# Performance work log

Measured on AMD Instinct MI355X. Metric: run time of the kernel, lower is better.

The kernel has to match this reference:

```python
import jax, jax.numpy as jnp
import numpy as np

KH = KW = 3
SH = SW = 1
PH = PW = 1
DH = DW = 1


def _median_pool2d(x):
    # x: (B, C, H, W); zero padding like F.unfold
    B, C, H, W = x.shape
    Ho = (H + 2 * PH - DH * (KH - 1) - 1) // SH + 1
    Wo = (W + 2 * PW - DW * (KW - 1) - 1) // SW + 1
    xp = jnp.pad(x, ((0, 0), (0, 0), (PH, PH), (PW, PW)))
    # gather kH*kW shifted strided views instead of materializing unfold copies per column
    wins = jnp.stack(
        [
            xp[:, :,
               i * DH: i * DH + (Ho - 1) * SH + 1: SH,
               j * DW: j * DW + (Wo - 1) * SW + 1: SW]
            for i in range(KH) for j in range(KW)
        ],
        axis=2,
    )  # (B, C, KH*KW, Ho, Wo)
    # torch.median returns the LOWER median: sorted element at index (n-1)//2
    s = jnp.sort(wins, axis=2)
    return s[:, :, (KH * KW - 1) // 2]


def setup_inputs() -> dict:
    key = jax.random.key(0)
    x = jax.random.normal(key, (8, 64, 256, 256), dtype=jnp.float32)
    return {"x": x}


def reference(x):
    return _median_pool2d(x)
```

## Files before the change

### kernel.cpp

```cpp
#include <hip/hip_runtime.h>
#include <hip/hip_bf16.h>


typedef float vf4 __attribute__((ext_vector_type(4)));

__device__ __forceinline__ float min3f(float a, float b, float c) {
    return fminf(fminf(a, b), c);
}
__device__ __forceinline__ float max3f(float a, float b, float c) {
    return fmaxf(fmaxf(a, b), c);
}
__device__ __forceinline__ float med3f(float a, float b, float c) {
    return __builtin_amdgcn_fmed3f(a, b, c);
}

__global__ __launch_bounds__(256)
void median3x3_kernel(const float* __restrict__ x, float* __restrict__ y, int total) {
    int idx = blockIdx.x * blockDim.x + threadIdx.x;
    if (idx >= total) return;

    const int w8 = idx & 31;
    const int hs = (idx >> 5) & 63;
    const int p  = idx >> 11;

    const float* plane = x + ((size_t)p << 16);
    const int c0 = w8 << 3;
    const int h0 = hs << 2;

    float r[6][10];
#pragma unroll
    for (int t = 0; t < 6; ++t) {
        const int hh = h0 + t - 1;
        vf4 a = (vf4)0.f;
        vf4 b = (vf4)0.f;
        if (hh >= 0 && hh <= 255) {
            const float* row = plane + (hh << 8);
            a = *reinterpret_cast<const vf4*>(row + c0);
            b = *reinterpret_cast<const vf4*>(row + c0 + 4);
        }
        r[t][1] = a.x; r[t][2] = a.y; r[t][3] = a.z; r[t][4] = a.w;
        r[t][5] = b.x; r[t][6] = b.y; r[t][7] = b.z; r[t][8] = b.w;
        const float left  = __shfl_up(b.w, 1);
        const float right = __shfl_down(a.x, 1);
        r[t][0] = (w8 == 0)  ? 0.f : left;
        r[t][9] = (w8 == 31) ? 0.f : right;
    }

    float* outbase = y + ((size_t)p << 16) + ((size_t)h0 << 8) + c0;

#pragma unroll
    for (int orow = 0; orow < 4; ++orow) {
        float lo[10], mi[10], hi[10];
#pragma unroll
        for (int j = 0; j < 10; ++j) {
            const float a = r[orow][j], b = r[orow + 1][j], c = r[orow + 2][j];
            lo[j] = min3f(a, b, c);
            mi[j] = med3f(a, b, c);
            hi[j] = max3f(a, b, c);
        }
        float res[8];
#pragma unroll
        for (int k = 0; k < 8; ++k) {
            const float A = max3f(lo[k], lo[k + 1], lo[k + 2]);
            const float B = med3f(mi[k], mi[k + 1], mi[k + 2]);
            const float C = min3f(hi[k], hi[k + 1], hi[k + 2]);
            res[k] = med3f(A, B, C);
        }
        float* out = outbase + (orow << 8);
        vf4 o0 = {res[0], res[1], res[2], res[3]};
        vf4 o1 = {res[4], res[5], res[6], res[7]};
        *reinterpret_cast<vf4*>(out)     = o0;
        *reinterpret_cast<vf4*>(out + 4) = o1;
    }
}

extern "C" void kernel_launch(void* const* d_in, const int* in_sizes, int n_in,
                              void* d_out, int out_size, void* d_ws, size_t ws_size,
                              hipStream_t stream) {
    const float* x = (const float*)d_in[0];
    float* y = (float*)d_out;
    const int total = out_size / 32;
    const int threads = 256;
    const int blocks = (total + threads - 1) / threads;
    median3x3_kernel<<<blocks, threads, 0, stream>>>(x, y, total);
}
```

Baseline: 47.12 us.

## Process eight planes per thread with double-buffered tile loads

Launches a fixed 512-block grid in which each thread walks eight planes strided by 64. Two register buffers let the next plane's loads be issued while the current plane's median is computed and stored. This aims to hide memory latency and amortise index arithmetic. In exchange, far fewer waves are resident and register pressure rises, which may reduce latency hiding in a bandwidth-bound kernel.

```diff
diff --git a/kernel.cpp b/kernel.cpp
--- a/kernel.cpp
+++ b/kernel.cpp
@@ -14,49 +14,43 @@
     return __builtin_amdgcn_fmed3f(a, b, c);
 }
 
-__global__ __launch_bounds__(256)
-void median3x3_kernel(const float* __restrict__ x, float* __restrict__ y, int total) {
-    int idx = blockIdx.x * blockDim.x + threadIdx.x;
-    if (idx >= total) return;
+__device__ __forceinline__ void load_tile(const float* __restrict__ plane,
+                                          int c0, int h0, bool topok, bool botok,
+                                          vf4 (&a)[6], vf4 (&b)[6]) {
+#pragma unroll
+    for (int t = 0; t < 6; ++t) {
+        const bool ok = (t == 0) ? topok : ((t == 5) ? botok : true);
+        vf4 va = (vf4)0.f, vb = (vf4)0.f;
+        if (ok) {
+            const float* row = plane + ((h0 + t - 1) << 8);
+            va = *reinterpret_cast<const vf4*>(row + c0);
+            vb = *reinterpret_cast<const vf4*>(row + c0 + 4);
+        }
+        a[t] = va; b[t] = vb;
+    }
+}
 
-    const int w8 = idx & 31;
-    const int hs = (idx >> 5) & 63;
-    const int p  = idx >> 11;
-
-    const float* plane = x + ((size_t)p << 16);
-    const int c0 = w8 << 3;
-    const int h0 = hs << 2;
-
+__device__ __forceinline__ void compute_store(const vf4 (&a)[6], const vf4 (&b)[6],
+                                              int w8, float* __restrict__ out) {
     float r[6][10];
 #pragma unroll
     for (int t = 0; t < 6; ++t) {
-        const int hh = h0 + t - 1;
-        vf4 a = (vf4)0.f;
-        vf4 b = (vf4)0.f;
-        if (hh >= 0 && hh <= 255) {
-            const float* row = plane + (hh << 8);
-            a = *reinterpret_cast<const vf4*>(row + c0);
-            b = *reinterpret_cast<const vf4*>(row + c0 + 4);
-        }
-        r[t][1] = a.x; r[t][2] = a.y; r[t][3] = a.z; r[t][4] = a.w;
-        r[t][5] = b.x; r[t][6] = b.y; r[t][7] = b.z; r[t][8] = b.w;
-        const float left  = __shfl_up(b.w, 1);
-        const float right = __shfl_down(a.x, 1);
+        r[t][1] = a[t].x; r[t][2] = a[t].y; r[t][3] = a[t].z; r[t][4] = a[t].w;
+        r[t][5] = b[t].x; r[t][6] = b[t].y; r[t][7] = b[t].z; r[t][8] = b[t].w;
+        const float left  = __shfl_up(b[t].w, 1);
+        const float right = __shfl_down(a[t].x, 1);
         r[t][0] = (w8 == 0)  ? 0.f : left;
         r[t][9] = (w8 == 31) ? 0.f : right;
     }
-
-    float* outbase = y + ((size_t)p << 16) + ((size_t)h0 << 8) + c0;
-
 #pragma unroll
     for (int orow = 0; orow < 4; ++orow) {
         float lo[10], mi[10], hi[10];
 #pragma unroll
         for (int j = 0; j < 10; ++j) {
-            const float a = r[orow][j], b = r[orow + 1][j], c = r[orow + 2][j];
-            lo[j] = min3f(a, b, c);
-            mi[j] = med3f(a, b, c);
-            hi[j] = max3f(a, b, c);
+            const float p = r[orow][j], q = r[orow + 1][j], s = r[orow + 2][j];
+            lo[j] = min3f(p, q, s);
+            mi[j] = med3f(p, q, s);
+            hi[j] = max3f(p, q, s);
         }
         float res[8];
 #pragma unroll
@@ -66,11 +60,38 @@
             const float C = min3f(hi[k], hi[k + 1], hi[k + 2]);
             res[k] = med3f(A, B, C);
         }
-        float* out = outbase + (orow << 8);
         vf4 o0 = {res[0], res[1], res[2], res[3]};
         vf4 o1 = {res[4], res[5], res[6], res[7]};
-        *reinterpret_cast<vf4*>(out)     = o0;
-        *reinterpret_cast<vf4*>(out + 4) = o1;
+        float* o = out + (orow << 8);
+        *reinterpret_cast<vf4*>(o)     = o0;
+        *reinterpret_cast<vf4*>(o + 4) = o1;
+    }
+}
+
+__global__ __launch_bounds__(256)
+void median3x3_kernel(const float* __restrict__ x, float* __restrict__ y) {
+    const int tid = blockIdx.x * 256 + threadIdx.x;
+    const int w8 = tid & 31;
+    const int hs = (tid >> 5) & 63;
+    const int p0 = tid >> 11;
+    const int c0 = w8 << 3;
+    const int h0 = hs << 2;
+    const bool topok = (hs > 0);
+    const bool botok = (hs < 63);
+
+    const size_t pstep = (size_t)64 << 16;
+    const float* xk = x + ((size_t)p0 << 16);
+    float* yk = y + ((size_t)p0 << 16) + ((size_t)h0 << 8) + c0;
+
+    vf4 aA[6], bA[6], aB[6], bB[6];
+    load_tile(xk, c0, h0, topok, botok, aA, bA);
+#pragma unroll
+    for (int k = 0; k < 8; k += 2) {
+        load_tile(xk + (size_t)(k + 1) * pstep, c0, h0, topok, botok, aB, bB);
+        compute_store(aA, bA, w8, yk + (size_t)k * pstep);
+        if (k + 2 < 8)
+            load_tile(xk + (size_t)(k + 2) * pstep, c0, h0, topok, botok, aA, bA);
+        compute_store(aB, bB, w8, yk + (size_t)(k + 1) * pstep);
     }
 }
 
@@ -79,8 +100,5 @@
                               hipStream_t stream) {
     const float* x = (const float*)d_in[0];
     float* y = (float*)d_out;
-    const int total = out_size / 32;
-    const int threads = 256;
-    const int blocks = (total + threads - 1) / threads;
-    median3x3_kernel<<<blocks, threads, 0, stream>>>(x, y, total);
+    median3x3_kernel<<<512, 256, 0, stream>>>(x, y);
 }
```

After: 46.07 us. 1.02x faster.
